# Performance work log

Hardware: AMD Instinct MI355X
Metric: run time of the kernel (lower is better)

Reference implementation:

```python
import jax, jax.numpy as jnp
import numpy as np

EPS = 1e-8  # torch.cosine_similarity default eps


def _gru_stack(x_seq, h0, w_ih, w_hh, b_ih, b_hh):
    """Multi-layer GRU with input_size=hidden_size=1, vectorized over N lanes.
    x_seq: [T, N], h0: [L, N], w_ih/w_hh/b_ih/b_hh: [L, 3] (gate order r, z, n).
    Returns (last-layer output seq [T, N], final hidden per layer [L, N])."""
    def layer_body(x_seq, p):
        wi, wh, bi, bh, h0_l = p
        def step(h, x):
            r = jax.nn.sigmoid(wi[0] * x + bi[0] + wh[0] * h + bh[0])
            z = jax.nn.sigmoid(wi[1] * x + bi[1] + wh[1] * h + bh[1])
            n = jnp.tanh(wi[2] * x + bi[2] + r * (wh[2] * h + bh[2]))
            h_new = (1.0 - z) * n + z * h
            return h_new, h_new
        h_fin, out = jax.lax.scan(step, h0_l, x_seq)
        return out, h_fin
    out_seq, h_fin = jax.lax.scan(layer_body, x_seq, (w_ih, w_hh, b_ih, b_hh, h0))
    return out_seq, h_fin


def _forward(inputs, w_ih, w_hh, b_ih, b_hh, horizon):
    B, _, nodes, T = inputs.shape
    L = w_ih.shape[0]  # == T (num_layers = seq_len)
    # [B,1,nodes,T] -> [T, nodes, B] -> [T, nodes*B]; GRU weights are shared
    # across nodes, so all per-node GRU calls batch into one.
    x = inputs[:, 0].transpose(2, 1, 0).reshape(T, nodes * B)
    h0 = jnp.zeros((L, nodes * B), inputs.dtype)
    out, h = _gru_stack(x, h0, w_ih, w_hh, b_ih, b_hh)
    # horizon-1 additional passes, feeding output back as input with carried h
    def hstep(carry, _):
        o, hh = carry
        o, hh = _gru_stack(o, hh, w_ih, w_hh, b_ih, b_hh)
        return (o, hh), None
    (out, h), _ = jax.lax.scan(hstep, (out, h), None, length=horizon - 1)
    hv = h.reshape(L, nodes, B)  # final hidden scalar per (layer, node, batch)
    # cosine similarity across the batch dim between every pair of nodes
    norms = jnp.maximum(jnp.linalg.norm(hv, axis=-1), EPS)  # [L, nodes]
    dots = jnp.einsum('lib,ljb->lij', hv, hv)               # [L, nodes, nodes]
    adj = dots / (norms[:, :, None] * norms[:, None, :])
    # h0_gru list-of-per-node tensors [L, B, 1] -> stacked [nodes, L, B, 1]
    h_out = hv.transpose(1, 0, 2)[..., None]
    return adj, h_out


def setup_inputs() -> dict:
    key = jax.random.key(0)
    ks = jax.random.split(key, 5)
    B, nodes, T, horizon = 16, 1024, 24, 8
    inputs = jax.random.normal(ks[0], (B, 1, nodes, T), dtype=jnp.float32)
    # PyTorch GRU init: U(-1/sqrt(hidden), 1/sqrt(hidden)) = U(-1, 1) here
    u = lambda k: jax.random.uniform(k, (T, 3), dtype=jnp.float32, minval=-1.0, maxval=1.0)
    return {"inputs": inputs, "w_ih": u(ks[1]), "w_hh": u(ks[2]),
            "b_ih": u(ks[3]), "b_hh": u(ks[4]), "horizon": horizon}


def reference(inputs, w_ih, w_hh, b_ih, b_hh, horizon):
    return _forward(inputs, w_ih, w_hh, b_ih, b_hh, horizon)
```

## Files before the change

kernel.cpp:

```cpp
#include <hip/hip_runtime.h>
#include <math.h>

#define NODES 1024
#define BATCH 16
#define TLEN 24
#define LAYERS 24
#define NLANES (NODES * BATCH)
#define LOG2E 1.44269504088896340736f
#define CPB 20

typedef float v2f __attribute__((ext_vector_type(2)));

#if __has_builtin(__builtin_amdgcn_rcpf)
__device__ __forceinline__ float fast_rcp(float x) { return __builtin_amdgcn_rcpf(x); }
#else
__device__ __forceinline__ float fast_rcp(float x) { return 1.0f / x; }
#endif

#if __has_builtin(__builtin_amdgcn_exp2f)
__device__ __forceinline__ float fast_exp2(float x) { return __builtin_amdgcn_exp2f(x); }
#else
__device__ __forceinline__ float fast_exp2(float x) { return exp2f(x); }
#endif

#if __has_builtin(__builtin_elementwise_fma)
__device__ __forceinline__ v2f pk_fma(v2f a, v2f b, v2f c) {
    return __builtin_elementwise_fma(a, b, c);
}
#else
__device__ __forceinline__ v2f pk_fma(v2f a, v2f b, v2f c) {
    v2f d; d.x = fmaf(a.x, b.x, c.x); d.y = fmaf(a.y, b.y, c.y); return d;
}
#endif

struct GruK {
    v2f rW, rU, rC, zW, zU, zC, nW, nC, nU, nD;
};

__device__ __forceinline__ GruK make_k2(
    const float* __restrict__ w_ih, const float* __restrict__ w_hh,
    const float* __restrict__ b_ih, const float* __restrict__ b_hh,
    int la, int lb)
{
    GruK K;
    #pragma unroll
    for (int s = 0; s < 2; ++s) {
        const int l = s ? lb : la;
        const float wi0 = w_ih[l*3+0], wi1 = w_ih[l*3+1], wi2 = w_ih[l*3+2];
        const float wh0 = w_hh[l*3+0], wh1 = w_hh[l*3+1], wh2 = w_hh[l*3+2];
        const float bi0 = b_ih[l*3+0], bi1 = b_ih[l*3+1], bi2 = b_ih[l*3+2];
        const float bh0 = b_hh[l*3+0], bh1 = b_hh[l*3+1], bh2 = b_hh[l*3+2];
        K.rW[s] = -LOG2E * wi0; K.rU[s] = -LOG2E * wh0; K.rC[s] = -LOG2E * (bi0 + bh0);
        K.zW[s] = -LOG2E * wi1; K.zU[s] = -LOG2E * wh1; K.zC[s] = -LOG2E * (bi1 + bh1);
        K.nW[s] = -2.0f*LOG2E * wi2; K.nC[s] = -2.0f*LOG2E * bi2;
        K.nU[s] = -2.0f*LOG2E * wh2; K.nD[s] = -2.0f*LOG2E * bh2;
    }
    return K;
}

__device__ __forceinline__ v2f gru_cell(const GruK& K, v2f h, v2f xin) {
    const v2f ONE = (v2f){1.0f, 1.0f};
    v2f ar = pk_fma(K.rU, h, pk_fma(K.rW, xin, K.rC));
    v2f az = pk_fma(K.zU, h, pk_fma(K.zW, xin, K.zC));
    v2f er; er.x = fast_exp2(ar.x); er.y = fast_exp2(ar.y);
    v2f ez; ez.x = fast_exp2(az.x); ez.y = fast_exp2(az.y);
    v2f er1 = er + ONE;
    v2f r;  r.x = fast_rcp(er1.x); r.y = fast_rcp(er1.y);
    v2f an = pk_fma(r, pk_fma(K.nU, h, K.nD), pk_fma(K.nW, xin, K.nC));
    v2f en; en.x = fast_exp2(an.x); en.y = fast_exp2(an.y);
    v2f num = pk_fma(en, h - ez, h + ez);
    v2f den = (ez + ONE) * (en + ONE);
    v2f rd; rd.x = fast_rcp(den.x); rd.y = fast_rcp(den.y);
    return num * rd;
}

__global__ __launch_bounds__(256) void gru_pipe_kernel(
    const float* __restrict__ inputs, const float* __restrict__ w_ih,
    const float* __restrict__ w_hh, const float* __restrict__ b_ih,
    const float* __restrict__ b_hh, const int* __restrict__ horizon_p,
    float* __restrict__ hv, float* __restrict__ h_out)
{
    __shared__ float xl[CPB][TLEN];
    const int tid = threadIdx.x;
    const int wid = tid >> 6;
    const int lane = tid & 63;
    const int r5 = lane / 12;
    const bool vlane = (lane < 60);
    const int ring = vlane ? r5 : 4;
    const int sl = vlane ? (lane - r5 * 12) : (lane - 60);
    const int c = blockIdx.x * CPB + wid * 5 + ring;
    const bool cvalid = vlane && (c < NLANES);

    const GruK K = make_k2(w_ih, w_hh, b_ih, b_hh, 2 * sl, 2 * sl + 1);

    for (int i = tid; i < CPB * TLEN; i += 256) {
        const int cl = i / TLEN, t = i - cl * TLEN;
        const int cc = blockIdx.x * CPB + cl;
        const int node = cc >> 4, b = cc & 15;
        xl[cl][t] = (cc < NLANES)
                  ? inputs[((size_t)b * NODES + node) * TLEN + t] : 0.0f;
    }
    __syncthreads();

    const int H = *horizon_p;
    const int last = H * TLEN;
    const int ringsrc = vlane
        ? (r5 * 12 + ((sl == 0) ? 11 : (sl - 1)))
        : lane;
    const bool lead = vlane && (sl == 0);
    const float* xrow = &xl[wid * 5 + ring][0];

    v2f h = (v2f){0.0f, 0.0f};

    for (int k = 0; k < TLEN; ++k) {
        v2f xin;
        xin.x = __shfl(h.y, ringsrc, 64);
        xin.y = h.x;
        if (lead) xin.x = xrow[k];
        v2f hn = gru_cell(K, h, xin);
        h.x = (k >= 2 * sl)     ? hn.x : h.x;
        h.y = (k >= 2 * sl + 1) ? hn.y : h.y;
    }
    for (int k = TLEN; k < last; ++k) {
        v2f xin;
        xin.x = __shfl(h.y, ringsrc, 64);
        xin.y = h.x;
        h = gru_cell(K, h, xin);
    }
    for (int k = last; k < last + LAYERS - 1; ++k) {
        v2f xin;
        xin.x = __shfl(h.y, ringsrc, 64);
        xin.y = h.x;
        v2f hn = gru_cell(K, h, xin);
        h.x = (k < 2 * sl + last)     ? hn.x : h.x;
        h.y = (k < 2 * sl + 1 + last) ? hn.y : h.y;
    }

    if (cvalid) {
        hv[(size_t)(2 * sl + 0) * NLANES + c] = h.x;
        hv[(size_t)(2 * sl + 1) * NLANES + c] = h.y;
        const int node = c >> 4, b = c & 15;
        float* ho = h_out + (size_t)node * (LAYERS * BATCH) + b;
        ho[(2 * sl + 0) * BATCH] = h.x;
        ho[(2 * sl + 1) * BATCH] = h.y;
    }
}

__global__ __launch_bounds__(256) void adj_kernel(
    const float* __restrict__ hv, float* __restrict__ adj)
{
    const int l = blockIdx.z;
    const int i0 = blockIdx.y * 64;
    const int j0 = blockIdx.x * 64;
    __shared__ float As[64 * 16];
    __shared__ float Bt[16 * 64];
    __shared__ float iA[64];
    __shared__ float iB[64];
    const int tid = threadIdx.x;
    const float* hvl = hv + (size_t)l * NLANES;

    ((float4*)As)[tid] = ((const float4*)(hvl + (size_t)i0 * 16))[tid];
    {
        const int j = tid >> 2;
        const int kc = (tid & 3) * 4;
        float4 bv = *(const float4*)(hvl + (size_t)(j0 + j) * 16 + kc);
        Bt[(kc + 0) * 64 + j] = bv.x;
        Bt[(kc + 1) * 64 + j] = bv.y;
        Bt[(kc + 2) * 64 + j] = bv.z;
        Bt[(kc + 3) * 64 + j] = bv.w;
    }
    __syncthreads();

    if (tid < 64) {
        float s = 0.0f;
        #pragma unroll
        for (int k = 0; k < 16; ++k) { float v = As[tid * 16 + k]; s = fmaf(v, v, s); }
        iA[tid] = fast_rcp(fmaxf(sqrtf(s), 1e-8f));
    } else if (tid < 128) {
        const int j = tid - 64;
        float s = 0.0f;
        #pragma unroll
        for (int k = 0; k < 16; ++k) { float v = Bt[k * 64 + j]; s = fmaf(v, v, s); }
        iB[j] = fast_rcp(fmaxf(sqrtf(s), 1e-8f));
    }
    __syncthreads();

    const int ty = tid >> 4;
    const int tx = tid & 15;

    float4 acc0 = {0,0,0,0}, acc1 = {0,0,0,0}, acc2 = {0,0,0,0}, acc3 = {0,0,0,0};
    #pragma unroll
    for (int kk = 0; kk < 4; ++kk) {
        float4 a0 = ((const float4*)As)[(ty * 4 + 0) * 4 + kk];
        float4 a1 = ((const float4*)As)[(ty * 4 + 1) * 4 + kk];
        float4 a2 = ((const float4*)As)[(ty * 4 + 2) * 4 + kk];
        float4 a3 = ((const float4*)As)[(ty * 4 + 3) * 4 + kk];
        #pragma unroll
        for (int e = 0; e < 4; ++e) {
            const int k = kk * 4 + e;
            float4 bk = ((const float4*)Bt)[k * 16 + tx];
            const float a0e = (e == 0) ? a0.x : (e == 1) ? a0.y : (e == 2) ? a0.z : a0.w;
            const float a1e = (e == 0) ? a1.x : (e == 1) ? a1.y : (e == 2) ? a1.z : a1.w;
            const float a2e = (e == 0) ? a2.x : (e == 1) ? a2.y : (e == 2) ? a2.z : a2.w;
            const float a3e = (e == 0) ? a3.x : (e == 1) ? a3.y : (e == 2) ? a3.z : a3.w;
            acc0.x = fmaf(a0e, bk.x, acc0.x); acc0.y = fmaf(a0e, bk.y, acc0.y);
            acc0.z = fmaf(a0e, bk.z, acc0.z); acc0.w = fmaf(a0e, bk.w, acc0.w);
            acc1.x = fmaf(a1e, bk.x, acc1.x); acc1.y = fmaf(a1e, bk.y, acc1.y);
            acc1.z = fmaf(a1e, bk.z, acc1.z); acc1.w = fmaf(a1e, bk.w, acc1.w);
            acc2.x = fmaf(a2e, bk.x, acc2.x); acc2.y = fmaf(a2e, bk.y, acc2.y);
            acc2.z = fmaf(a2e, bk.z, acc2.z); acc2.w = fmaf(a2e, bk.w, acc2.w);
            acc3.x = fmaf(a3e, bk.x, acc3.x); acc3.y = fmaf(a3e, bk.y, acc3.y);
            acc3.z = fmaf(a3e, bk.z, acc3.z); acc3.w = fmaf(a3e, bk.w, acc3.w);
        }
    }

    float* out = adj + (size_t)l * NODES * NODES;
    const float4 ib4 = ((const float4*)iB)[tx];
    #pragma unroll
    for (int ii = 0; ii < 4; ++ii) {
        const int i = i0 + ty * 4 + ii;
        const float si = iA[ty * 4 + ii];
        float4 a = (ii == 0) ? acc0 : (ii == 1) ? acc1 : (ii == 2) ? acc2 : acc3;
        float4 w;
        w.x = a.x * si * ib4.x;
        w.y = a.y * si * ib4.y;
        w.z = a.z * si * ib4.z;
        w.w = a.w * si * ib4.w;
        *(float4*)(out + (size_t)i * NODES + j0 + tx * 4) = w;
    }
}

extern "C" void kernel_launch(void* const* d_in, const int* in_sizes, int n_in,
                              void* d_out, int out_size, void* d_ws, size_t ws_size,
                              hipStream_t stream) {
    const float* inputs = (const float*)d_in[0];
    const float* w_ih   = (const float*)d_in[1];
    const float* w_hh   = (const float*)d_in[2];
    const float* b_ih   = (const float*)d_in[3];
    const float* b_hh   = (const float*)d_in[4];
    const int*   horiz  = (const int*)d_in[5];

    float* adj   = (float*)d_out;
    float* h_out = (float*)d_out + (size_t)LAYERS * NODES * NODES;
    float* hv    = (float*)d_ws;

    const int nblk = (NLANES + CPB - 1) / CPB;
    gru_pipe_kernel<<<nblk, 256, 0, stream>>>(inputs, w_ih, w_hh, b_ih, b_hh,
                                              horiz, hv, h_out);

    dim3 grid(NODES / 64, NODES / 64, LAYERS);
    adj_kernel<<<grid, 256, 0, stream>>>(hv, adj);
}
```

Measured before the change: 88.12 us.

## Assign six GRU layers per lane with four-lane rings per chain

The layer-pipelined GRU mapping changes from 12 lanes per chain (2 layers each, 60 of 64 lanes used) to 4 lanes per chain, each holding 6 layers in three packed pairs. This removes the idle lanes and cuts cross-lane shuffles to one per three cells, and each lane now has three independent cell chains for instruction-level parallelism. In exchange, register pressure per lane rises, the grid shrinks to 256 blocks, and the warm-up and drain steps are longer per chain. The shared input tile is padded to avoid bank conflicts, and the middle loop is unrolled.

```diff
diff --git a/kernel.cpp b/kernel.cpp
--- a/kernel.cpp
+++ b/kernel.cpp
@@ -7,7 +7,6 @@
 #define LAYERS 24
 #define NLANES (NODES * BATCH)
 #define LOG2E 1.44269504088896340736f
-#define CPB 20
 
 typedef float v2f __attribute__((ext_vector_type(2)));
 
@@ -80,70 +79,85 @@
     const float* __restrict__ b_hh, const int* __restrict__ horizon_p,
     float* __restrict__ hv, float* __restrict__ h_out)
 {
-    __shared__ float xl[CPB][TLEN];
+    __shared__ float xl[64][TLEN + 1];
     const int tid = threadIdx.x;
     const int wid = tid >> 6;
     const int lane = tid & 63;
-    const int r5 = lane / 12;
-    const bool vlane = (lane < 60);
-    const int ring = vlane ? r5 : 4;
-    const int sl = vlane ? (lane - r5 * 12) : (lane - 60);
-    const int c = blockIdx.x * CPB + wid * 5 + ring;
-    const bool cvalid = vlane && (c < NLANES);
-
-    const GruK K = make_k2(w_ih, w_hh, b_ih, b_hh, 2 * sl, 2 * sl + 1);
-
-    for (int i = tid; i < CPB * TLEN; i += 256) {
+    const int ring = lane >> 2;
+    const int sl = lane & 3;
+    const int L0 = 6 * sl;
+    const int chain_local = wid * 16 + ring;
+    const int c = blockIdx.x * 64 + chain_local;
+
+    const GruK K0 = make_k2(w_ih, w_hh, b_ih, b_hh, L0 + 0, L0 + 1);
+    const GruK K1 = make_k2(w_ih, w_hh, b_ih, b_hh, L0 + 2, L0 + 3);
+    const GruK K2 = make_k2(w_ih, w_hh, b_ih, b_hh, L0 + 4, L0 + 5);
+
+    for (int i = tid; i < 64 * TLEN; i += 256) {
         const int cl = i / TLEN, t = i - cl * TLEN;
-        const int cc = blockIdx.x * CPB + cl;
+        const int cc = blockIdx.x * 64 + cl;
         const int node = cc >> 4, b = cc & 15;
-        xl[cl][t] = (cc < NLANES)
-                  ? inputs[((size_t)b * NODES + node) * TLEN + t] : 0.0f;
+        xl[cl][t] = inputs[((size_t)b * NODES + node) * TLEN + t];
     }
     __syncthreads();
 
     const int H = *horizon_p;
     const int last = H * TLEN;
-    const int ringsrc = vlane
-        ? (r5 * 12 + ((sl == 0) ? 11 : (sl - 1)))
-        : lane;
-    const bool lead = vlane && (sl == 0);
-    const float* xrow = &xl[wid * 5 + ring][0];
-
-    v2f h = (v2f){0.0f, 0.0f};
+    const int ringsrc = (lane & 60) | ((sl + 3) & 3);
+    const bool lead = (sl == 0);
+    const float* xrow = &xl[chain_local][0];
+
+    v2f h0 = (v2f){0.0f, 0.0f}, h1 = h0, h2 = h0;
 
     for (int k = 0; k < TLEN; ++k) {
-        v2f xin;
-        xin.x = __shfl(h.y, ringsrc, 64);
-        xin.y = h.x;
-        if (lead) xin.x = xrow[k];
-        v2f hn = gru_cell(K, h, xin);
-        h.x = (k >= 2 * sl)     ? hn.x : h.x;
-        h.y = (k >= 2 * sl + 1) ? hn.y : h.y;
-    }
+        float rel = __shfl(h2.y, ringsrc, 64);
+        v2f in0; in0.x = lead ? xrow[k] : rel; in0.y = h0.x;
+        v2f in1; in1.x = h0.y; in1.y = h1.x;
+        v2f in2; in2.x = h1.y; in2.y = h2.x;
+        v2f n0 = gru_cell(K0, h0, in0);
+        v2f n1 = gru_cell(K1, h1, in1);
+        v2f n2 = gru_cell(K2, h2, in2);
+        h0.x = (k >= L0 + 0) ? n0.x : h0.x;
+        h0.y = (k >= L0 + 1) ? n0.y : h0.y;
+        h1.x = (k >= L0 + 2) ? n1.x : h1.x;
+        h1.y = (k >= L0 + 3) ? n1.y : h1.y;
+        h2.x = (k >= L0 + 4) ? n2.x : h2.x;
+        h2.y = (k >= L0 + 5) ? n2.y : h2.y;
+    }
+    #pragma unroll 4
     for (int k = TLEN; k < last; ++k) {
-        v2f xin;
-        xin.x = __shfl(h.y, ringsrc, 64);
-        xin.y = h.x;
-        h = gru_cell(K, h, xin);
+        float rel = __shfl(h2.y, ringsrc, 64);
+        v2f in2; in2.x = h1.y; in2.y = h2.x;
+        v2f in1; in1.x = h0.y; in1.y = h1.x;
+        v2f in0; in0.x = rel;  in0.y = h0.x;
+        h2 = gru_cell(K2, h2, in2);
+        h1 = gru_cell(K1, h1, in1);
+        h0 = gru_cell(K0, h0, in0);
     }
     for (int k = last; k < last + LAYERS - 1; ++k) {
-        v2f xin;
-        xin.x = __shfl(h.y, ringsrc, 64);
-        xin.y = h.x;
-        v2f hn = gru_cell(K, h, xin);
-        h.x = (k < 2 * sl + last)     ? hn.x : h.x;
-        h.y = (k < 2 * sl + 1 + last) ? hn.y : h.y;
-    }
-
-    if (cvalid) {
-        hv[(size_t)(2 * sl + 0) * NLANES + c] = h.x;
-        hv[(size_t)(2 * sl + 1) * NLANES + c] = h.y;
-        const int node = c >> 4, b = c & 15;
-        float* ho = h_out + (size_t)node * (LAYERS * BATCH) + b;
-        ho[(2 * sl + 0) * BATCH] = h.x;
-        ho[(2 * sl + 1) * BATCH] = h.y;
-    }
+        float rel = __shfl(h2.y, ringsrc, 64);
+        v2f in0; in0.x = rel;  in0.y = h0.x;
+        v2f in1; in1.x = h0.y; in1.y = h1.x;
+        v2f in2; in2.x = h1.y; in2.y = h2.x;
+        v2f n0 = gru_cell(K0, h0, in0);
+        v2f n1 = gru_cell(K1, h1, in1);
+        v2f n2 = gru_cell(K2, h2, in2);
+        h0.x = (k < L0 + 0 + last) ? n0.x : h0.x;
+        h0.y = (k < L0 + 1 + last) ? n0.y : h0.y;
+        h1.x = (k < L0 + 2 + last) ? n1.x : h1.x;
+        h1.y = (k < L0 + 3 + last) ? n1.y : h1.y;
+        h2.x = (k < L0 + 4 + last) ? n2.x : h2.x;
+        h2.y = (k < L0 + 5 + last) ? n2.y : h2.y;
+    }
+
+    const int node = c >> 4, b = c & 15;
+    float* ho = h_out + (size_t)node * (LAYERS * BATCH) + b;
+    hv[(size_t)(L0 + 0) * NLANES + c] = h0.x;  ho[(L0 + 0) * BATCH] = h0.x;
+    hv[(size_t)(L0 + 1) * NLANES + c] = h0.y;  ho[(L0 + 1) * BATCH] = h0.y;
+    hv[(size_t)(L0 + 2) * NLANES + c] = h1.x;  ho[(L0 + 2) * BATCH] = h1.x;
+    hv[(size_t)(L0 + 3) * NLANES + c] = h1.y;  ho[(L0 + 3) * BATCH] = h1.y;
+    hv[(size_t)(L0 + 4) * NLANES + c] = h2.x;  ho[(L0 + 4) * BATCH] = h2.x;
+    hv[(size_t)(L0 + 5) * NLANES + c] = h2.y;  ho[(L0 + 5) * BATCH] = h2.y;
 }
 
 __global__ __launch_bounds__(256) void adj_kernel(
@@ -244,9 +258,8 @@
     float* h_out = (float*)d_out + (size_t)LAYERS * NODES * NODES;
     float* hv    = (float*)d_ws;
 
-    const int nblk = (NLANES + CPB - 1) / CPB;
-    gru_pipe_kernel<<<nblk, 256, 0, stream>>>(inputs, w_ih, w_hh, b_ih, b_hh,
-                                              horiz, hv, h_out);
+    gru_pipe_kernel<<<NLANES / 64, 256, 0, stream>>>(inputs, w_ih, w_hh, b_ih, b_hh,
+                                                     horiz, hv, h_out);
 
     dim3 grid(NODES / 64, NODES / 64, LAYERS);
     adj_kernel<<<grid, 256, 0, stream>>>(hv, adj);
```

Result: faster. 80.90 us (-8.2%).

## Map three GRU layers per lane with 8-lane rings per chain

Applied to the files above, without the earlier changes.

The wavefront pipeline is restructured so each lane handles three consecutive layers (a packed pair plus a scalar) and eight lanes form a ring per chain. This replaces the previous two-layers-per-lane layout, where 12-lane rings left 4 of 64 lanes idle. Each wave now processes 8 chains instead of 5, with 32 chains per block and no bounds checks. The cost is a longer per-step dependency chain, since each lane's three cells are partly serial and the scalar cell does not use packed math. The change also adds padding to the shared input tile and unrolls the steady-state loop.

```diff
diff --git a/kernel.cpp b/kernel.cpp
--- a/kernel.cpp
+++ b/kernel.cpp
@@ -7,7 +7,6 @@
 #define LAYERS 24
 #define NLANES (NODES * BATCH)
 #define LOG2E 1.44269504088896340736f
-#define CPB 20
 
 typedef float v2f __attribute__((ext_vector_type(2)));
 
@@ -33,32 +32,43 @@
 }
 #endif
 
-struct GruK {
-    v2f rW, rU, rC, zW, zU, zC, nW, nC, nU, nD;
-};
-
-__device__ __forceinline__ GruK make_k2(
+struct GruK2 { v2f rW, rU, rC, zW, zU, zC, nW, nC, nU, nD; };
+struct GruKs { float rW, rU, rC, zW, zU, zC, nW, nC, nU, nD; };
+
+__device__ __forceinline__ GruK2 make_k2(
     const float* __restrict__ w_ih, const float* __restrict__ w_hh,
     const float* __restrict__ b_ih, const float* __restrict__ b_hh,
     int la, int lb)
 {
-    GruK K;
+    GruK2 K;
     #pragma unroll
     for (int s = 0; s < 2; ++s) {
         const int l = s ? lb : la;
-        const float wi0 = w_ih[l*3+0], wi1 = w_ih[l*3+1], wi2 = w_ih[l*3+2];
-        const float wh0 = w_hh[l*3+0], wh1 = w_hh[l*3+1], wh2 = w_hh[l*3+2];
-        const float bi0 = b_ih[l*3+0], bi1 = b_ih[l*3+1], bi2 = b_ih[l*3+2];
-        const float bh0 = b_hh[l*3+0], bh1 = b_hh[l*3+1], bh2 = b_hh[l*3+2];
-        K.rW[s] = -LOG2E * wi0; K.rU[s] = -LOG2E * wh0; K.rC[s] = -LOG2E * (bi0 + bh0);
-        K.zW[s] = -LOG2E * wi1; K.zU[s] = -LOG2E * wh1; K.zC[s] = -LOG2E * (bi1 + bh1);
-        K.nW[s] = -2.0f*LOG2E * wi2; K.nC[s] = -2.0f*LOG2E * bi2;
-        K.nU[s] = -2.0f*LOG2E * wh2; K.nD[s] = -2.0f*LOG2E * bh2;
+        K.rW[s] = -LOG2E * w_ih[l*3+0]; K.rU[s] = -LOG2E * w_hh[l*3+0];
+        K.rC[s] = -LOG2E * (b_ih[l*3+0] + b_hh[l*3+0]);
+        K.zW[s] = -LOG2E * w_ih[l*3+1]; K.zU[s] = -LOG2E * w_hh[l*3+1];
+        K.zC[s] = -LOG2E * (b_ih[l*3+1] + b_hh[l*3+1]);
+        K.nW[s] = -2.0f*LOG2E * w_ih[l*3+2]; K.nC[s] = -2.0f*LOG2E * b_ih[l*3+2];
+        K.nU[s] = -2.0f*LOG2E * w_hh[l*3+2]; K.nD[s] = -2.0f*LOG2E * b_hh[l*3+2];
     }
     return K;
 }
 
-__device__ __forceinline__ v2f gru_cell(const GruK& K, v2f h, v2f xin) {
+__device__ __forceinline__ GruKs make_ks(
+    const float* __restrict__ w_ih, const float* __restrict__ w_hh,
+    const float* __restrict__ b_ih, const float* __restrict__ b_hh, int l)
+{
+    GruKs K;
+    K.rW = -LOG2E * w_ih[l*3+0]; K.rU = -LOG2E * w_hh[l*3+0];
+    K.rC = -LOG2E * (b_ih[l*3+0] + b_hh[l*3+0]);
+    K.zW = -LOG2E * w_ih[l*3+1]; K.zU = -LOG2E * w_hh[l*3+1];
+    K.zC = -LOG2E * (b_ih[l*3+1] + b_hh[l*3+1]);
+    K.nW = -2.0f*LOG2E * w_ih[l*3+2]; K.nC = -2.0f*LOG2E * b_ih[l*3+2];
+    K.nU = -2.0f*LOG2E * w_hh[l*3+2]; K.nD = -2.0f*LOG2E * b_hh[l*3+2];
+    return K;
+}
+
+__device__ __forceinline__ v2f gru_cell2(const GruK2& K, v2f h, v2f xin) {
     const v2f ONE = (v2f){1.0f, 1.0f};
     v2f ar = pk_fma(K.rU, h, pk_fma(K.rW, xin, K.rC));
     v2f az = pk_fma(K.zU, h, pk_fma(K.zW, xin, K.zC));
@@ -74,76 +84,89 @@
     return num * rd;
 }
 
+__device__ __forceinline__ float gru_cells(const GruKs& K, float h, float xin) {
+    float ar = fmaf(K.rU, h, fmaf(K.rW, xin, K.rC));
+    float az = fmaf(K.zU, h, fmaf(K.zW, xin, K.zC));
+    float er = fast_exp2(ar);
+    float ez = fast_exp2(az);
+    float r  = fast_rcp(1.0f + er);
+    float an = fmaf(r, fmaf(K.nU, h, K.nD), fmaf(K.nW, xin, K.nC));
+    float en = fast_exp2(an);
+    float num = fmaf(en, h - ez, h + ez);
+    float den = (1.0f + ez) * (1.0f + en);
+    return num * fast_rcp(den);
+}
+
 __global__ __launch_bounds__(256) void gru_pipe_kernel(
     const float* __restrict__ inputs, const float* __restrict__ w_ih,
     const float* __restrict__ w_hh, const float* __restrict__ b_ih,
     const float* __restrict__ b_hh, const int* __restrict__ horizon_p,
     float* __restrict__ hv, float* __restrict__ h_out)
 {
-    __shared__ float xl[CPB][TLEN];
+    __shared__ float xl[32][TLEN + 1];
     const int tid = threadIdx.x;
     const int wid = tid >> 6;
     const int lane = tid & 63;
-    const int r5 = lane / 12;
-    const bool vlane = (lane < 60);
-    const int ring = vlane ? r5 : 4;
-    const int sl = vlane ? (lane - r5 * 12) : (lane - 60);
-    const int c = blockIdx.x * CPB + wid * 5 + ring;
-    const bool cvalid = vlane && (c < NLANES);
-
-    const GruK K = make_k2(w_ih, w_hh, b_ih, b_hh, 2 * sl, 2 * sl + 1);
-
-    for (int i = tid; i < CPB * TLEN; i += 256) {
+    const int ring = lane >> 3;
+    const int sl = lane & 7;
+    const int L0 = 3 * sl;
+    const int chain_local = wid * 8 + ring;
+    const int c = blockIdx.x * 32 + chain_local;
+
+    const GruK2 K01 = make_k2(w_ih, w_hh, b_ih, b_hh, L0, L0 + 1);
+    const GruKs K2  = make_ks(w_ih, w_hh, b_ih, b_hh, L0 + 2);
+
+    for (int i = tid; i < 32 * TLEN; i += 256) {
         const int cl = i / TLEN, t = i - cl * TLEN;
-        const int cc = blockIdx.x * CPB + cl;
+        const int cc = blockIdx.x * 32 + cl;
         const int node = cc >> 4, b = cc & 15;
-        xl[cl][t] = (cc < NLANES)
-                  ? inputs[((size_t)b * NODES + node) * TLEN + t] : 0.0f;
+        xl[cl][t] = inputs[((size_t)b * NODES + node) * TLEN + t];
     }
     __syncthreads();
 
     const int H = *horizon_p;
     const int last = H * TLEN;
-    const int ringsrc = vlane
-        ? (r5 * 12 + ((sl == 0) ? 11 : (sl - 1)))
-        : lane;
-    const bool lead = vlane && (sl == 0);
-    const float* xrow = &xl[wid * 5 + ring][0];
-
-    v2f h = (v2f){0.0f, 0.0f};
+    const int ringsrc = (lane & 56) | ((sl + 7) & 7);
+    const bool lead = (sl == 0);
+    const float* xrow = &xl[chain_local][0];
+
+    v2f h01 = (v2f){0.0f, 0.0f};
+    float h2 = 0.0f;
 
     for (int k = 0; k < TLEN; ++k) {
-        v2f xin;
-        xin.x = __shfl(h.y, ringsrc, 64);
-        xin.y = h.x;
-        if (lead) xin.x = xrow[k];
-        v2f hn = gru_cell(K, h, xin);
-        h.x = (k >= 2 * sl)     ? hn.x : h.x;
-        h.y = (k >= 2 * sl + 1) ? hn.y : h.y;
-    }
+        float rel = __shfl(h2, ringsrc, 64);
+        v2f in01; in01.x = lead ? xrow[k] : rel; in01.y = h01.x;
+        float p1 = h01.y;
+        v2f n01 = gru_cell2(K01, h01, in01);
+        float n2 = gru_cells(K2, h2, p1);
+        h01.x = (k >= L0 + 0) ? n01.x : h01.x;
+        h01.y = (k >= L0 + 1) ? n01.y : h01.y;
+        h2    = (k >= L0 + 2) ? n2   : h2;
+    }
+    #pragma unroll 4
     for (int k = TLEN; k < last; ++k) {
-        v2f xin;
-        xin.x = __shfl(h.y, ringsrc, 64);
-        xin.y = h.x;
-        h = gru_cell(K, h, xin);
+        float rel = __shfl(h2, ringsrc, 64);
+        float p1 = h01.y;
+        v2f in01; in01.x = rel; in01.y = h01.x;
+        h2  = gru_cells(K2, h2, p1);
+        h01 = gru_cell2(K01, h01, in01);
     }
     for (int k = last; k < last + LAYERS - 1; ++k) {
-        v2f xin;
-        xin.x = __shfl(h.y, ringsrc, 64);
-        xin.y = h.x;
-        v2f hn = gru_cell(K, h, xin);
-        h.x = (k < 2 * sl + last)     ? hn.x : h.x;
-        h.y = (k < 2 * sl + 1 + last) ? hn.y : h.y;
-    }
-
-    if (cvalid) {
-        hv[(size_t)(2 * sl + 0) * NLANES + c] = h.x;
-        hv[(size_t)(2 * sl + 1) * NLANES + c] = h.y;
-        const int node = c >> 4, b = c & 15;
-        float* ho = h_out + (size_t)node * (LAYERS * BATCH) + b;
-        ho[(2 * sl + 0) * BATCH] = h.x;
-        ho[(2 * sl + 1) * BATCH] = h.y;
-    }
+        float rel = __shfl(h2, ringsrc, 64);
+        v2f in01; in01.x = rel; in01.y = h01.x;
+        float p1 = h01.y;
+        v2f n01 = gru_cell2(K01, h01, in01);
+        float n2 = gru_cells(K2, h2, p1);
+        h01.x = (k < L0 + 0 + last) ? n01.x : h01.x;
+        h01.y = (k < L0 + 1 + last) ? n01.y : h01.y;
+        h2    = (k < L0 + 2 + last) ? n2   : h2;
+    }
+
+    const int node = c >> 4, b = c & 15;
+    float* ho = h_out + (size_t)node * (LAYERS * BATCH) + b;
+    hv[(size_t)(L0 + 0) * NLANES + c] = h01.x;  ho[(L0 + 0) * BATCH] = h01.x;
+    hv[(size_t)(L0 + 1) * NLANES + c] = h01.y;  ho[(L0 + 1) * BATCH] = h01.y;
+    hv[(size_t)(L0 + 2) * NLANES + c] = h2;     ho[(L0 + 2) * BATCH] = h2;
 }
 
 __global__ __launch_bounds__(256) void adj_kernel(
@@ -244,9 +267,8 @@
     float* h_out = (float*)d_out + (size_t)LAYERS * NODES * NODES;
     float* hv    = (float*)d_ws;
 
-    const int nblk = (NLANES + CPB - 1) / CPB;
-    gru_pipe_kernel<<<nblk, 256, 0, stream>>>(inputs, w_ih, w_hh, b_ih, b_hh,
-                                              horiz, hv, h_out);
+    gru_pipe_kernel<<<NLANES / 32, 256, 0, stream>>>(inputs, w_ih, w_hh, b_ih, b_hh,
+                                                     horiz, hv, h_out);
 
     dim3 grid(NODES / 64, NODES / 64, LAYERS);
     adj_kernel<<<grid, 256, 0, stream>>>(hv, adj);
```

Result: faster. 76.95 us (-12.7%).
